# Kernel optimization log

Hardware: AMD Instinct MI355X
Metric: run time of the kernel (lower is better)

The kernel has to match this reference:

```python
import jax, jax.numpy as jnp
import numpy as np


def setup_inputs() -> dict:
    key = jax.random.key(0)
    k1, k2 = jax.random.split(key)
    inputs = jax.random.normal(k1, (4, 128, 64, 64), dtype=jnp.float32)
    # binary hole mask (1 = known background, 0 = hole), broadcast over channels
    mask = jnp.round(jax.random.uniform(k2, (4, 1, 64, 64), dtype=jnp.float32))
    return {"inputs": inputs, "mask": mask}


def reference(inputs, mask):
    # SFFA contextual attention with 1x1 dynamic kernels.
    # Note: in the original torch code the 1x1 conv with padding=1 produces
    # border scores that conv_transpose2d with padding=1 crops away exactly,
    # so the math reduces to per-pixel matmul + softmax + matmul.
    bz, nc, h, w = inputs.shape
    N = h * w
    background = inputs * mask                              # [b, c, h, w]
    # dynamic kernels: one nc-dim vector per background pixel (patch)
    K = background.reshape(bz, nc, N).transpose(0, 2, 1) + 1e-7   # [b, N, c]
    Kn = K / jnp.sqrt(jnp.sum(K * K, axis=2, keepdims=True))      # l2-normalized
    feat = inputs.reshape(bz, nc, N)                        # [b, c, N]
    scores = jnp.einsum('bpc,bcn->bpn', Kn, feat)           # [b, N(patch), N(pixel)]
    attn = jax.nn.softmax(scores, axis=1)                   # softmax over patches p
    agg = jnp.einsum('bpc,bpn->bcn', K, attn).reshape(bz, nc, h, w)
    return background + agg * (1.0 - mask)
```

## Files before the change

kernel.cpp:

```cpp
#include <hip/hip_runtime.h>
#include <hip/hip_bf16.h>

typedef __attribute__((ext_vector_type(8))) short bf16x8;
typedef __attribute__((ext_vector_type(4))) float f32x4;

#define NPIX 4096
#define NC   128
#define RS128 0.08838834764831845f

__global__ __launch_bounds__(1024) void sffa_prep(
    const float* __restrict__ x, const float* __restrict__ mask,
    ushort* __restrict__ KnW, ushort* __restrict__ QW, ushort* __restrict__ VtW,
    float* __restrict__ s0c, int* __restrict__ pixQ, int* __restrict__ cnts,
    float* __restrict__ out)
{
    __shared__ float xs[128][69];
    __shared__ float ms[64];
    __shared__ float rinv[64];
    __shared__ float ssum[64];
    __shared__ float2 part[16][64];
    __shared__ int se[64];
    __shared__ int bgn[64];
    __shared__ int tinfo[2];
    __shared__ int wredP[16], wredT[16];
    const int tid = threadIdx.x;
    const int b = blockIdx.x >> 6, nblk = blockIdx.x & 63;
    const int n0 = nblk * 64;
    const float* xb = x + (size_t)b * NC * NPIX;
    float* ob = out + (size_t)b * NC * NPIX;

    #pragma unroll
    for (int it = 0; it < 2; ++it) {
        int e4 = it * 1024 + tid;
        int c = e4 >> 4, n4 = (e4 & 15) * 4;
        float4 v = *(const float4*)(xb + (size_t)c * NPIX + n0 + n4);
        xs[c][n4+0] = v.x; xs[c][n4+1] = v.y; xs[c][n4+2] = v.z; xs[c][n4+3] = v.w;
        *(float4*)(ob + (size_t)c * NPIX + n0 + n4) = v;
    }
    if (tid < 16) {
        float4 mv = *(const float4*)(mask + (size_t)b * NPIX + n0 + tid * 4);
        ms[tid*4+0] = mv.x; ms[tid*4+1] = mv.y; ms[tid*4+2] = mv.z; ms[tid*4+3] = mv.w;
    }
    {
        const int lane = tid & 63, w = tid >> 6;
        float4 mv = *(const float4*)(mask + (size_t)b * NPIX + tid * 4);
        int f0 = mv.x < 0.5f ? 0x10000 : 1;
        int f1 = mv.y < 0.5f ? 0x10000 : 1;
        int f2 = mv.z < 0.5f ? 0x10000 : 1;
        int f3 = mv.w < 0.5f ? 0x10000 : 1;
        int p0 = tid * 4;
        int pre = 0, tot = f0 + f1 + f2 + f3;
        if (p0 + 0 < n0) pre += f0;
        if (p0 + 1 < n0) pre += f1;
        if (p0 + 2 < n0) pre += f2;
        if (p0 + 3 < n0) pre += f3;
        #pragma unroll
        for (int d = 1; d < 64; d <<= 1) {
            pre += __shfl_xor(pre, d);
            tot += __shfl_xor(tot, d);
        }
        if (lane == 0) { wredP[w] = pre; wredT[w] = tot; }
    }
    __syncthreads();
    if (tid < 64) {
        int vP = (tid < 16) ? wredP[tid] : 0;
        int vT = (tid < 16) ? wredT[tid] : 0;
        #pragma unroll
        for (int d = 1; d < 16; d <<= 1) {
            vP += __shfl_xor(vP, d);
            vT += __shfl_xor(vT, d);
        }
        int base  = __shfl(vP, 0);
        int total = __shfl(vT, 0);
        if (tid == 0 && nblk == 0) {
            cnts[b * 2]     = total & 0xffff;
            cnts[b * 2 + 1] = total >> 16;
        }
        int f = ms[tid] > 0.5f ? 1 : 0x10000;
        int s = f;
        #pragma unroll
        for (int d = 1; d < 64; d <<= 1) {
            int t = __shfl_up(s, d);
            if (tid >= d) s += t;
        }
        se[tid] = base + s - f;
    }
    __syncthreads();
    {
        int p = tid & 63, qd = tid >> 6;
        float m = ms[p];
        float s2 = 0.f, s1 = 0.f;
        #pragma unroll
        for (int i = 0; i < 8; ++i) {
            float xv = xs[qd*8 + i][p];
            float k = fmaf(xv, m, 1e-7f);
            s2 = fmaf(k, k, s2);
            s1 += xv;
        }
        part[qd][p] = make_float2(s2, s1);
    }
    __syncthreads();
    if (tid < 64) {
        float s2 = 0.f, s1 = 0.f;
        #pragma unroll
        for (int k = 0; k < 16; ++k) { float2 t = part[k][tid]; s2 += t.x; s1 += t.y; }
        rinv[tid] = rsqrtf(s2);
        ssum[tid] = s1 * RS128;
    }
    __syncthreads();
    #pragma unroll
    for (int it = 0; it < 4; ++it) {
        int e2 = it * 1024 + tid;
        int n = e2 >> 6, cp = (e2 & 63) * 2;
        int pe = se[n];
        float x0 = xs[cp][n], x1 = xs[cp+1][n];
        if (ms[n] > 0.5f) {
            int slot = pe & 0xffff;
            float k0 = x0 + 1e-7f, k1 = x1 + 1e-7f;
            float r = rinv[n];
            __hip_bfloat162 kn;
            kn.x = __float2bfloat16(k0 * r); kn.y = __float2bfloat16(k1 * r);
            *(__hip_bfloat162*)(KnW + ((size_t)b * NPIX + slot) * NC + cp) = kn;
        } else {
            int slot = pe >> 16;
            __hip_bfloat162 q;
            q.x = __float2bfloat16(x0); q.y = __float2bfloat16(x1);
            *(__hip_bfloat162*)(QW + ((size_t)b * NPIX + slot) * NC + cp) = q;
        }
    }
    if (tid < 64) {
        if (ms[tid] < 0.5f) {
            int slot = se[tid] >> 16;
            s0c [(size_t)b * NPIX + slot] = ssum[tid];
            pixQ[(size_t)b * NPIX + slot] = n0 + tid;
        } else {
            bgn[(se[tid] & 0xffff) - (se[0] & 0xffff)] = tid;
        }
    }
    if (tid == 0) {
        tinfo[0] = se[0] & 0xffff;
        tinfo[1] = (se[63] & 0xffff) + (ms[63] > 0.5f ? 1 : 0) - (se[0] & 0xffff);
    }
    __syncthreads();
    {
        const int s0b = tinfo[0], nbg = tinfo[1];
        const int j = tid & 63, cg = tid >> 6;
        if (j < nbg) {
            int n = bgn[j];
            ushort* vcol = VtW + (size_t)b * NC * NPIX + s0b + j;
            #pragma unroll
            for (int cc = 0; cc < 8; ++cc) {
                int c = cg * 8 + cc;
                __hip_bfloat16 h = __float2bfloat16(xs[c][n] + 1e-7f);
                vcol[(size_t)c * NPIX] = *(ushort*)&h;
            }
        }
    }
}

#define L_BUF 32768
#define L_P   65536
#define L_ML  75776
#define L_SZ  76800

__global__ __launch_bounds__(512, 4) void sffa_attn(
    const ushort* __restrict__ KnW, const ushort* __restrict__ QW,
    const ushort* __restrict__ VtW, const int* __restrict__ cnts,
    ushort* __restrict__ partW, float* __restrict__ mlW, int KS)
{
    __shared__ __align__(16) char smem[L_SZ];
    const int tid  = threadIdx.x;
    const int w = tid >> 6, lane = tid & 63;
    const int l15 = lane & 15, g = lane >> 4;
    const int bx = (int)blockIdx.x;
    const int per = 64 * KS;
    const int b = bx / per;
    const int rem = bx - b * per;
    const int qblk = rem / KS, ks = rem - (rem / KS) * KS;
    const int q0 = qblk * 64;
    const int cntK = cnts[b * 2], cntQ = cnts[b * 2 + 1];
    if (q0 >= cntQ) return;
    const int blk = (b * 64 + qblk) * KS + ks;

    const int nk64 = (cntK + 63) >> 6;
    const int tpk  = (nk64 + KS - 1) / KS;
    const int t0   = ks * tpk;
    const int t1   = min(t0 + tpk, nk64);
    const int NTK  = t1 - t0;

    if (NTK <= 0) {
        unsigned* pz = (unsigned*)(partW + (size_t)blk * 8192);
        #pragma unroll
        for (int i = 0; i < 8; ++i) pz[i * 512 + tid] = 0u;
        if (tid < 64)
            *(float2*)(mlW + ((size_t)blk * 64 + tid) * 2) = make_float2(-1e30f, 0.f);
        return;
    }

    const int half = w >> 2;
    const int wq   = w & 3;
    const int kbase = t0 * 64;

    const ushort* Knb = KnW + (size_t)b * NPIX * NC;
    const ushort* Qb  = QW  + (size_t)b * NPIX * NC + (size_t)q0 * NC;
    const ushort* Vtb = VtW + (size_t)b * NC * NPIX;

    #pragma unroll
    for (int it = 0; it < 2; ++it) {
        int L = (it * 512 + tid) * 16;
        int row = L >> 8, col = L & 255;
        int4 v = *(const int4*)((const char*)Qb + L);
        *(int4*)(smem + row * 256 + (col ^ ((row & 15) << 4))) = v;
    }
    __syncthreads();
    bf16x8 qf[4];
    {
        int qrow = wq * 16 + l15;
        #pragma unroll
        for (int kc = 0; kc < 4; ++kc)
            qf[kc] = *(const bf16x8*)(smem + qrow * 256 + ((64*kc + 16*g) ^ (l15 << 4)));
    }
    __syncthreads();

    const int kOff = (tid >> 4) * 256 + (((tid & 15) * 16) ^ (((tid >> 4) & 15) << 4));
    const int cV = tid >> 3, sV = tid & 7;
    const int vOff = cV * 128 + ((sV * 16) ^ ((cV & 7) << 4));
    const int4* kgbase = (const int4*)(Knb + (size_t)kbase * NC);
    const ushort* vgbase = Vtb + (size_t)cV * NPIX + kbase + sV * 8;

    int4 pr0, pr1, pr2, pr3;
    pr0 = kgbase[tid]; pr1 = kgbase[512 + tid];
    pr2 = *(const int4*)(vgbase);
    pr3 = *(const int4*)(vgbase + (size_t)64 * NPIX);
    {
        char* base = smem;
        *(int4*)(base + kOff) = pr0;
        *(int4*)(base + kOff + 8192) = pr1;
        *(int4*)(base + 16384 + vOff) = pr2;
        *(int4*)(base + 16384 + vOff + 8192) = pr3;
    }
    if (NTK > 1) {
        pr0 = kgbase[1024 + tid]; pr1 = kgbase[1536 + tid];
        pr2 = *(const int4*)(vgbase + 64);
        pr3 = *(const int4*)(vgbase + (size_t)64 * NPIX + 64);
    }
    __syncthreads();

    f32x4 acc[8];
    const f32x4 fzero = {0.f, 0.f, 0.f, 0.f};
    #pragma unroll
    for (int i = 0; i < 8; ++i) acc[i] = fzero;
    float mrun = -1e30f, lrun = 0.f;
    char* Pw = smem + L_P + w * 1280;

    for (int kt = 0; kt < NTK; ++kt) {
        if (kt + 1 < NTK) {
            char* base = smem + ((kt + 1) & 1) * L_BUF;
            *(int4*)(base + kOff) = pr0;
            *(int4*)(base + kOff + 8192) = pr1;
            *(int4*)(base + 16384 + vOff) = pr2;
            *(int4*)(base + 16384 + vOff + 8192) = pr3;
        }
        if (kt + 2 < NTK) {
            pr0 = kgbase[(kt + 2) * 1024 + tid];
            pr1 = kgbase[(kt + 2) * 1024 + 512 + tid];
            pr2 = *(const int4*)(vgbase + (kt + 2) * 64);
            pr3 = *(const int4*)(vgbase + (size_t)64 * NPIX + (kt + 2) * 64);
        }
        char* bb = smem + (kt & 1) * L_BUF;
        f32x4 sa0 = fzero, sa1 = fzero;
        {
            const char* rb0 = bb + (half * 32 + l15) * 256;
            const char* rb1 = rb0 + 4096;
            const int sw = l15 << 4;
            __builtin_amdgcn_s_setprio(1);
            #pragma unroll
            for (int kc = 0; kc < 4; ++kc) {
                int off = (64 * kc + 16 * g) ^ sw;
                bf16x8 a0 = *(const bf16x8*)(rb0 + off);
                bf16x8 a1 = *(const bf16x8*)(rb1 + off);
                sa0 = __builtin_amdgcn_mfma_f32_16x16x32_bf16(a0, qf[kc], sa0, 0, 0, 0);
                sa1 = __builtin_amdgcn_mfma_f32_16x16x32_bf16(a1, qf[kc], sa1, 0, 0, 0);
            }
            __builtin_amdgcn_s_setprio(0);
        }
        {
            int kg0 = (t0 + kt) * 64;
            if (kg0 + 64 > cntK) {
                int kb = cntK - kg0;
                int kr = half * 32 + 4 * g;
                #pragma unroll
                for (int r = 0; r < 4; ++r) {
                    if (kr + r >= kb)      sa0[r] = -3e38f;
                    if (kr + 16 + r >= kb) sa1[r] = -3e38f;
                }
            }
        }
        float tmax = fmaxf(fmaxf(fmaxf(sa0[0], sa0[1]), fmaxf(sa0[2], sa0[3])),
                           fmaxf(fmaxf(sa1[0], sa1[1]), fmaxf(sa1[2], sa1[3])));
        tmax = fmaxf(tmax, __shfl_xor(tmax, 16));
        tmax = fmaxf(tmax, __shfl_xor(tmax, 32));
        bool grow = !__all(tmax <= mrun + 8.f);
        float mnew = grow ? fmaxf(mrun, tmax) : mrun;
        float p0[4], p1[4];
        float ts = 0.f;
        #pragma unroll
        for (int r = 0; r < 4; ++r) { p0[r] = __expf(sa0[r] - mnew); ts += p0[r]; }
        #pragma unroll
        for (int r = 0; r < 4; ++r) { p1[r] = __expf(sa1[r] - mnew); ts += p1[r]; }
        ts += __shfl_xor(ts, 16);
        ts += __shfl_xor(ts, 32);
        if (grow) {
            float sc = __expf(mrun - mnew);
            lrun = lrun * sc + ts;
            float scr[4];
            #pragma unroll
            for (int r = 0; r < 4; ++r) scr[r] = __shfl(sc, 4 * g + r);
            #pragma unroll
            for (int ct = 0; ct < 8; ++ct) {
                acc[ct][0] *= scr[0]; acc[ct][1] *= scr[1];
                acc[ct][2] *= scr[2]; acc[ct][3] *= scr[3];
            }
            mrun = mnew;
        } else {
            lrun += ts;
        }
        union { __hip_bfloat162 h; unsigned u; } ua0, ua1, ub0, ub1;
        ua0.h.x = __float2bfloat16(p0[0]); ua0.h.y = __float2bfloat16(p0[1]);
        ua1.h.x = __float2bfloat16(p0[2]); ua1.h.y = __float2bfloat16(p0[3]);
        ub0.h.x = __float2bfloat16(p1[0]); ub0.h.y = __float2bfloat16(p1[1]);
        ub1.h.x = __float2bfloat16(p1[2]); ub1.h.y = __float2bfloat16(p1[3]);
        *(int2*)(Pw + l15 * 80 +      8 * g) = make_int2((int)ua0.u, (int)ua1.u);
        *(int2*)(Pw + l15 * 80 + 32 + 8 * g) = make_int2((int)ub0.u, (int)ub1.u);
        bf16x8 pf = *(const bf16x8*)(Pw + l15 * 80 + 16 * g);
        {
            const char* vb = bb + 16384;
            __builtin_amdgcn_s_setprio(1);
            #pragma unroll
            for (int ct = 0; ct < 8; ++ct) {
                int c = 16 * ct + l15;
                bf16x8 vf = *(const bf16x8*)(vb + c * 128 +
                                             ((64 * half + 16 * g) ^ ((c & 7) << 4)));
                acc[ct] = __builtin_amdgcn_mfma_f32_16x16x32_bf16(pf, vf, acc[ct], 0, 0, 0);
            }
            __builtin_amdgcn_s_setprio(0);
        }
        __syncthreads();
    }

    float* ma = (float*)(smem + L_ML);
    float* la = ma + 64; float* mb = la + 64; float* lb = mb + 64;
    const int q = wq * 16 + l15;
    if (g == 0) {
        if (half == 0) { ma[q] = mrun; la[q] = lrun; }
        else           { mb[q] = mrun; lb[q] = lrun; }
    }
    __syncthreads();
    float* agg = (float*)smem;
    {
        float mstar = fmaxf(ma[q], mb[q]);
        float f = __expf(mrun - mstar);
        float fr[4];
        #pragma unroll
        for (int r = 0; r < 4; ++r) fr[r] = __shfl(f, 4 * g + r);
        if (half == 1) {
            #pragma unroll
            for (int ct = 0; ct < 8; ++ct) {
                int c = 16 * ct + l15;
                #pragma unroll
                for (int r = 0; r < 4; ++r)
                    agg[c * 68 + wq * 16 + 4 * g + r] = acc[ct][r] * fr[r];
            }
        }
        __syncthreads();
        if (half == 0) {
            #pragma unroll
            for (int ct = 0; ct < 8; ++ct) {
                int c = 16 * ct + l15;
                #pragma unroll
                for (int r = 0; r < 4; ++r) {
                    int idx = c * 68 + wq * 16 + 4 * g + r;
                    agg[idx] = acc[ct][r] * fr[r] + agg[idx];
                }
            }
        }
    }
    __syncthreads();
    if (tid < 64) {
        float M = fmaxf(ma[tid], mb[tid]);
        float ls = la[tid] * __expf(ma[tid] - M) + lb[tid] * __expf(mb[tid] - M);
        *(float2*)(mlW + ((size_t)blk * 64 + tid) * 2) = make_float2(M, ls);
    }
    ushort* pdst = partW + (size_t)blk * 8192;
    #pragma unroll
    for (int it = 0; it < 8; ++it) {
        int idx = it * 512 + tid;
        int c = idx >> 5, n2 = (idx & 31) * 2;
        __hip_bfloat162 h;
        h.x = __float2bfloat16(agg[c * 68 + n2]);
        h.y = __float2bfloat16(agg[c * 68 + n2 + 1]);
        *(__hip_bfloat162*)(pdst + c * 64 + n2) = h;
    }
}

__global__ __launch_bounds__(256) void sffa_comb(
    const ushort* __restrict__ partW, const float* __restrict__ mlW,
    const float* __restrict__ s0c, const int* __restrict__ pixQ,
    const int* __restrict__ cnts, float* __restrict__ out, int KS)
{
    __shared__ float wgtL[4][64];
    __shared__ int pixnL[64];
    const int tid = threadIdx.x;
    const int bx = blockIdx.x;
    const int b = bx >> 8, qb = (bx >> 2) & 63, ch = bx & 3;
    const int cntK = cnts[b * 2], cntQ = cnts[b * 2 + 1];
    if (qb * 64 >= cntQ) return;
    const int blkbase = (b * 64 + qb) * KS;
    const float m0f = (float)(NPIX - cntK);

    if (tid < 64) {
        int slot = qb * 64 + tid;
        int pix = -1;
        if (slot < cntQ) {
            pix = pixQ[(size_t)b * NPIX + slot];
            float s0 = s0c[(size_t)b * NPIX + slot];
            float M = s0;
            float2 mls[4];
            #pragma unroll
            for (int k = 0; k < 4; ++k) {
                if (k < KS) {
                    mls[k] = *(const float2*)(mlW + ((size_t)(blkbase + k) * 64 + tid) * 2);
                    M = fmaxf(M, mls[k].x);
                }
            }
            float L = m0f * __expf(s0 - M);
            #pragma unroll
            for (int k = 0; k < 4; ++k)
                if (k < KS) L += mls[k].y * __expf(mls[k].x - M);
            float Li = 1.f / L;
            #pragma unroll
            for (int k = 0; k < 4; ++k)
                if (k < KS) wgtL[k][tid] = __expf(mls[k].x - M) * Li;
        }
        pixnL[tid] = pix;
    }
    __syncthreads();

    float* ob = out + (size_t)b * NC * NPIX;
    const ushort* pb = partW + (size_t)blkbase * 8192;
    {
        int cl = tid >> 3, grp = tid & 7;
        int c = ch * 32 + cl;
        float v[8] = {0.f,0.f,0.f,0.f,0.f,0.f,0.f,0.f};
        #pragma unroll
        for (int k = 0; k < 4; ++k) {
            if (k < KS) {
                ushort u[8];
                *(int4*)u = *(const int4*)(pb + (size_t)k * 8192 + c * 64 + grp * 8);
                #pragma unroll
                for (int j = 0; j < 8; ++j)
                    v[j] = fmaf(__uint_as_float((unsigned)u[j] << 16),
                                wgtL[k][grp * 8 + j], v[j]);
            }
        }
        #pragma unroll
        for (int j = 0; j < 8; ++j) {
            int pix = pixnL[grp * 8 + j];
            if (pix >= 0) ob[(size_t)c * NPIX + pix] = v[j];
        }
    }
}

extern "C" void kernel_launch(void* const* d_in, const int* in_sizes, int n_in,
                              void* d_out, int out_size, void* d_ws, size_t ws_size,
                              hipStream_t stream) {
    const float* x    = (const float*)d_in[0];
    const float* mask = (const float*)d_in[1];
    char* ws = (char*)d_ws;
    const size_t MBy = 1024 * 1024;
    const size_t KBy = 1024;

    ushort* KnW = (ushort*)(ws);
    ushort* QW  = (ushort*)(ws + 4 * MBy);
    ushort* VtW = (ushort*)(ws + 8 * MBy);

    size_t need4 = 12 * MBy + 4 * 4 * MBy + 1 * MBy;
    int KS = (ws_size >= need4) ? 4 : 2;
    ushort* partW = (ushort*)(ws + 12 * MBy);
    char* tail = ws + 12 * MBy + (size_t)KS * 4 * MBy;
    float* mlW    = (float*)(tail);
    float* s0c    = (float*)(tail + 576 * KBy);
    int*   pixQ   = (int*)(tail + 640 * KBy);
    int*   cnts   = (int*)(tail + 704 * KBy);

    sffa_prep <<<256, 1024, 0, stream>>>(x, mask, KnW, QW, VtW, s0c, pixQ, cnts,
                                         (float*)d_out);
    sffa_attn <<<4 * 64 * KS, 512, 0, stream>>>(KnW, QW, VtW, cnts, partW, mlW, KS);
    sffa_comb <<<4 * 64 * 4, 256, 0, stream>>>(partW, mlW, s0c, pixQ, cnts,
                                               (float*)d_out, KS);
}
```

Before: 53.38 us.

## Halve attention query tile to 32 rows, single-buffer LDS, 256-thread blocks

The attention kernel now handles 32 queries per block with 256 threads instead of 64 queries with 512. It replaces the double-buffered K/V shared memory with a single buffer refilled from registers after a barrier, and loads Q fragments straight from global memory without staging them in LDS. The goal is to cut LDS use roughly in half and double the block count, so more blocks fit per CU and the 256 CUs are better filled. The cost is that each K/V tile is loaded by twice as many blocks, and there is an extra barrier per tile with no overlap between the LDS write and compute. The combine kernel is reshaped to match the 32-query partials.

```diff
diff --git a/kernel.cpp b/kernel.cpp
--- a/kernel.cpp
+++ b/kernel.cpp
@@ -158,12 +158,12 @@
     }
 }
 
-#define L_BUF 32768
-#define L_P   65536
-#define L_ML  75776
-#define L_SZ  76800
-
-__global__ __launch_bounds__(512, 4) void sffa_attn(
+#define L_V   16384
+#define L_P   32768
+#define L_ML  37888
+#define L_SZ  38400
+
+__global__ __launch_bounds__(256, 4) void sffa_attn(
     const ushort* __restrict__ KnW, const ushort* __restrict__ QW,
     const ushort* __restrict__ VtW, const int* __restrict__ cnts,
     ushort* __restrict__ partW, float* __restrict__ mlW, int KS)
@@ -173,78 +173,71 @@
     const int w = tid >> 6, lane = tid & 63;
     const int l15 = lane & 15, g = lane >> 4;
     const int bx = (int)blockIdx.x;
-    const int per = 64 * KS;
+    const int per = 128 * KS;
     const int b = bx / per;
     const int rem = bx - b * per;
     const int qblk = rem / KS, ks = rem - (rem / KS) * KS;
-    const int q0 = qblk * 64;
+    const int q0 = qblk * 32;
     const int cntK = cnts[b * 2], cntQ = cnts[b * 2 + 1];
     if (q0 >= cntQ) return;
-    const int blk = (b * 64 + qblk) * KS + ks;
+    const int blk = (b * 128 + qblk) * KS + ks;
 
     const int nk64 = (cntK + 63) >> 6;
     const int tpk  = (nk64 + KS - 1) / KS;
     const int t0   = ks * tpk;
-    const int t1   = min(t0 + tpk, nk64);
-    const int NTK  = t1 - t0;
+    const int NTK  = min(t0 + tpk, nk64) - t0;
 
     if (NTK <= 0) {
-        unsigned* pz = (unsigned*)(partW + (size_t)blk * 8192);
-        #pragma unroll
-        for (int i = 0; i < 8; ++i) pz[i * 512 + tid] = 0u;
-        if (tid < 64)
-            *(float2*)(mlW + ((size_t)blk * 64 + tid) * 2) = make_float2(-1e30f, 0.f);
+        int4 z = {0,0,0,0};
+        int4* pz = (int4*)(partW + (size_t)blk * 4096);
+        pz[tid] = z; pz[256 + tid] = z;
+        if (tid < 32)
+            *(float2*)(mlW + ((size_t)blk * 32 + tid) * 2) = make_float2(-1e30f, 0.f);
         return;
     }
 
-    const int half = w >> 2;
-    const int wq   = w & 3;
+    const int wq = w & 1;
+    const int kh = w >> 1;
     const int kbase = t0 * 64;
 
     const ushort* Knb = KnW + (size_t)b * NPIX * NC;
-    const ushort* Qb  = QW  + (size_t)b * NPIX * NC + (size_t)q0 * NC;
     const ushort* Vtb = VtW + (size_t)b * NC * NPIX;
 
-    #pragma unroll
-    for (int it = 0; it < 2; ++it) {
-        int L = (it * 512 + tid) * 16;
-        int row = L >> 8, col = L & 255;
-        int4 v = *(const int4*)((const char*)Qb + L);
-        *(int4*)(smem + row * 256 + (col ^ ((row & 15) << 4))) = v;
-    }
-    __syncthreads();
     bf16x8 qf[4];
     {
-        int qrow = wq * 16 + l15;
+        const ushort* Qrow = QW + ((size_t)b * NPIX + q0 + wq * 16 + l15) * NC;
         #pragma unroll
         for (int kc = 0; kc < 4; ++kc)
-            qf[kc] = *(const bf16x8*)(smem + qrow * 256 + ((64*kc + 16*g) ^ (l15 << 4)));
-    }
-    __syncthreads();
+            qf[kc] = *(const bf16x8*)(Qrow + 32 * kc + 8 * g);
+    }
 
     const int kOff = (tid >> 4) * 256 + (((tid & 15) * 16) ^ (((tid >> 4) & 15) << 4));
-    const int cV = tid >> 3, sV = tid & 7;
-    const int vOff = cV * 128 + ((sV * 16) ^ ((cV & 7) << 4));
-    const int4* kgbase = (const int4*)(Knb + (size_t)kbase * NC);
-    const ushort* vgbase = Vtb + (size_t)cV * NPIX + kbase + sV * 8;
-
-    int4 pr0, pr1, pr2, pr3;
-    pr0 = kgbase[tid]; pr1 = kgbase[512 + tid];
-    pr2 = *(const int4*)(vgbase);
-    pr3 = *(const int4*)(vgbase + (size_t)64 * NPIX);
-    {
-        char* base = smem;
-        *(int4*)(base + kOff) = pr0;
-        *(int4*)(base + kOff + 8192) = pr1;
-        *(int4*)(base + 16384 + vOff) = pr2;
-        *(int4*)(base + 16384 + vOff + 8192) = pr3;
-    }
+    const int vOff = (tid >> 3) * 128 + (((tid & 7) * 16) ^ (((tid >> 3) & 7) << 4));
+    const int4* kg = (const int4*)(Knb + (size_t)kbase * NC);
+    const ushort* vg = Vtb + (size_t)(tid >> 3) * NPIX + kbase + (tid & 7) * 8;
+
+    int4 prK0, prK1, prK2, prK3, prV0, prV1, prV2, prV3;
+    prK0 = kg[tid]; prK1 = kg[256+tid]; prK2 = kg[512+tid]; prK3 = kg[768+tid];
+    prV0 = *(const int4*)(vg);
+    prV1 = *(const int4*)(vg + (size_t)32 * NPIX);
+    prV2 = *(const int4*)(vg + (size_t)64 * NPIX);
+    prV3 = *(const int4*)(vg + (size_t)96 * NPIX);
+    *(int4*)(smem + kOff)          = prK0;
+    *(int4*)(smem + kOff + 4096)   = prK1;
+    *(int4*)(smem + kOff + 8192)   = prK2;
+    *(int4*)(smem + kOff + 12288)  = prK3;
+    *(int4*)(smem + L_V + vOff)         = prV0;
+    *(int4*)(smem + L_V + vOff + 4096)  = prV1;
+    *(int4*)(smem + L_V + vOff + 8192)  = prV2;
+    *(int4*)(smem + L_V + vOff + 12288) = prV3;
+    __syncthreads();
     if (NTK > 1) {
-        pr0 = kgbase[1024 + tid]; pr1 = kgbase[1536 + tid];
-        pr2 = *(const int4*)(vgbase + 64);
-        pr3 = *(const int4*)(vgbase + (size_t)64 * NPIX + 64);
-    }
-    __syncthreads();
+        prK0 = kg[1024+tid]; prK1 = kg[1280+tid]; prK2 = kg[1536+tid]; prK3 = kg[1792+tid];
+        prV0 = *(const int4*)(vg + 64);
+        prV1 = *(const int4*)(vg + (size_t)32 * NPIX + 64);
+        prV2 = *(const int4*)(vg + (size_t)64 * NPIX + 64);
+        prV3 = *(const int4*)(vg + (size_t)96 * NPIX + 64);
+    }
 
     f32x4 acc[8];
     const f32x4 fzero = {0.f, 0.f, 0.f, 0.f};
@@ -254,23 +247,9 @@
     char* Pw = smem + L_P + w * 1280;
 
     for (int kt = 0; kt < NTK; ++kt) {
-        if (kt + 1 < NTK) {
-            char* base = smem + ((kt + 1) & 1) * L_BUF;
-            *(int4*)(base + kOff) = pr0;
-            *(int4*)(base + kOff + 8192) = pr1;
-            *(int4*)(base + 16384 + vOff) = pr2;
-            *(int4*)(base + 16384 + vOff + 8192) = pr3;
-        }
-        if (kt + 2 < NTK) {
-            pr0 = kgbase[(kt + 2) * 1024 + tid];
-            pr1 = kgbase[(kt + 2) * 1024 + 512 + tid];
-            pr2 = *(const int4*)(vgbase + (kt + 2) * 64);
-            pr3 = *(const int4*)(vgbase + (size_t)64 * NPIX + (kt + 2) * 64);
-        }
-        char* bb = smem + (kt & 1) * L_BUF;
         f32x4 sa0 = fzero, sa1 = fzero;
         {
-            const char* rb0 = bb + (half * 32 + l15) * 256;
+            const char* rb0 = smem + (kh * 32 + l15) * 256;
             const char* rb1 = rb0 + 4096;
             const int sw = l15 << 4;
             __builtin_amdgcn_s_setprio(1);
@@ -288,7 +267,7 @@
             int kg0 = (t0 + kt) * 64;
             if (kg0 + 64 > cntK) {
                 int kb = cntK - kg0;
-                int kr = half * 32 + 4 * g;
+                int kr = kh * 32 + 4 * g;
                 #pragma unroll
                 for (int r = 0; r < 4; ++r) {
                     if (kr + r >= kb)      sa0[r] = -3e38f;
@@ -334,72 +313,90 @@
         *(int2*)(Pw + l15 * 80 + 32 + 8 * g) = make_int2((int)ub0.u, (int)ub1.u);
         bf16x8 pf = *(const bf16x8*)(Pw + l15 * 80 + 16 * g);
         {
-            const char* vb = bb + 16384;
+            const char* bv = smem + L_V;
             __builtin_amdgcn_s_setprio(1);
             #pragma unroll
             for (int ct = 0; ct < 8; ++ct) {
                 int c = 16 * ct + l15;
-                bf16x8 vf = *(const bf16x8*)(vb + c * 128 +
-                                             ((64 * half + 16 * g) ^ ((c & 7) << 4)));
+                bf16x8 vf = *(const bf16x8*)(bv + c * 128 +
+                                             ((64 * kh + 16 * g) ^ ((c & 7) << 4)));
                 acc[ct] = __builtin_amdgcn_mfma_f32_16x16x32_bf16(pf, vf, acc[ct], 0, 0, 0);
             }
             __builtin_amdgcn_s_setprio(0);
         }
         __syncthreads();
+        if (kt + 1 < NTK) {
+            *(int4*)(smem + kOff)          = prK0;
+            *(int4*)(smem + kOff + 4096)   = prK1;
+            *(int4*)(smem + kOff + 8192)   = prK2;
+            *(int4*)(smem + kOff + 12288)  = prK3;
+            *(int4*)(smem + L_V + vOff)         = prV0;
+            *(int4*)(smem + L_V + vOff + 4096)  = prV1;
+            *(int4*)(smem + L_V + vOff + 8192)  = prV2;
+            *(int4*)(smem + L_V + vOff + 12288) = prV3;
+            __syncthreads();
+            if (kt + 2 < NTK) {
+                int tb = (kt + 2) * 1024;
+                prK0 = kg[tb+tid]; prK1 = kg[tb+256+tid];
+                prK2 = kg[tb+512+tid]; prK3 = kg[tb+768+tid];
+                const ushort* vgk = vg + (kt + 2) * 64;
+                prV0 = *(const int4*)(vgk);
+                prV1 = *(const int4*)(vgk + (size_t)32 * NPIX);
+                prV2 = *(const int4*)(vgk + (size_t)64 * NPIX);
+                prV3 = *(const int4*)(vgk + (size_t)96 * NPIX);
+            }
+        }
     }
 
     float* ma = (float*)(smem + L_ML);
-    float* la = ma + 64; float* mb = la + 64; float* lb = mb + 64;
-    const int q = wq * 16 + l15;
-    if (g == 0) {
-        if (half == 0) { ma[q] = mrun; la[q] = lrun; }
-        else           { mb[q] = mrun; lb[q] = lrun; }
-    }
+    float* la = ma + 64;
+    const int qs = wq * 16 + l15;
+    if (g == 0) { ma[kh * 32 + qs] = mrun; la[kh * 32 + qs] = lrun; }
     __syncthreads();
     float* agg = (float*)smem;
     {
-        float mstar = fmaxf(ma[q], mb[q]);
+        float mstar = fmaxf(ma[qs], ma[32 + qs]);
         float f = __expf(mrun - mstar);
         float fr[4];
         #pragma unroll
         for (int r = 0; r < 4; ++r) fr[r] = __shfl(f, 4 * g + r);
-        if (half == 1) {
+        if (kh == 1) {
             #pragma unroll
             for (int ct = 0; ct < 8; ++ct) {
                 int c = 16 * ct + l15;
                 #pragma unroll
                 for (int r = 0; r < 4; ++r)
-                    agg[c * 68 + wq * 16 + 4 * g + r] = acc[ct][r] * fr[r];
+                    agg[c * 36 + wq * 16 + 4 * g + r] = acc[ct][r] * fr[r];
             }
         }
         __syncthreads();
-        if (half == 0) {
+        if (kh == 0) {
             #pragma unroll
             for (int ct = 0; ct < 8; ++ct) {
                 int c = 16 * ct + l15;
                 #pragma unroll
                 for (int r = 0; r < 4; ++r) {
-                    int idx = c * 68 + wq * 16 + 4 * g + r;
+                    int idx = c * 36 + wq * 16 + 4 * g + r;
                     agg[idx] = acc[ct][r] * fr[r] + agg[idx];
                 }
             }
         }
     }
     __syncthreads();
-    if (tid < 64) {
-        float M = fmaxf(ma[tid], mb[tid]);
-        float ls = la[tid] * __expf(ma[tid] - M) + lb[tid] * __expf(mb[tid] - M);
-        *(float2*)(mlW + ((size_t)blk * 64 + tid) * 2) = make_float2(M, ls);
-    }
-    ushort* pdst = partW + (size_t)blk * 8192;
+    if (tid < 32) {
+        float M = fmaxf(ma[tid], ma[32 + tid]);
+        float ls = la[tid] * __expf(ma[tid] - M) + la[32 + tid] * __expf(ma[32 + tid] - M);
+        *(float2*)(mlW + ((size_t)blk * 32 + tid) * 2) = make_float2(M, ls);
+    }
+    ushort* pdst = partW + (size_t)blk * 4096;
     #pragma unroll
     for (int it = 0; it < 8; ++it) {
-        int idx = it * 512 + tid;
-        int c = idx >> 5, n2 = (idx & 31) * 2;
+        int idx = it * 256 + tid;
+        int c = idx >> 4, n2 = (idx & 15) * 2;
         __hip_bfloat162 h;
-        h.x = __float2bfloat16(agg[c * 68 + n2]);
-        h.y = __float2bfloat16(agg[c * 68 + n2 + 1]);
-        *(__hip_bfloat162*)(pdst + c * 64 + n2) = h;
+        h.x = __float2bfloat16(agg[c * 36 + n2]);
+        h.y = __float2bfloat16(agg[c * 36 + n2 + 1]);
+        *(__hip_bfloat162*)(pdst + c * 32 + n2) = h;
     }
 }
 
@@ -408,18 +405,18 @@
     const float* __restrict__ s0c, const int* __restrict__ pixQ,
     const int* __restrict__ cnts, float* __restrict__ out, int KS)
 {
-    __shared__ float wgtL[4][64];
-    __shared__ int pixnL[64];
+    __shared__ float wgtL[4][32];
+    __shared__ int pixnL[32];
     const int tid = threadIdx.x;
     const int bx = blockIdx.x;
-    const int b = bx >> 8, qb = (bx >> 2) & 63, ch = bx & 3;
+    const int b = bx >> 7, qb = bx & 127;
     const int cntK = cnts[b * 2], cntQ = cnts[b * 2 + 1];
-    if (qb * 64 >= cntQ) return;
-    const int blkbase = (b * 64 + qb) * KS;
+    if (qb * 32 >= cntQ) return;
+    const int blkbase = (b * 128 + qb) * KS;
     const float m0f = (float)(NPIX - cntK);
 
-    if (tid < 64) {
-        int slot = qb * 64 + tid;
+    if (tid < 32) {
+        int slot = qb * 32 + tid;
         int pix = -1;
         if (slot < cntQ) {
             pix = pixQ[(size_t)b * NPIX + slot];
@@ -429,7 +426,7 @@
             #pragma unroll
             for (int k = 0; k < 4; ++k) {
                 if (k < KS) {
-                    mls[k] = *(const float2*)(mlW + ((size_t)(blkbase + k) * 64 + tid) * 2);
+                    mls[k] = *(const float2*)(mlW + ((size_t)(blkbase + k) * 32 + tid) * 2);
                     M = fmaxf(M, mls[k].x);
                 }
             }
@@ -447,25 +444,27 @@
     __syncthreads();
 
     float* ob = out + (size_t)b * NC * NPIX;
-    const ushort* pb = partW + (size_t)blkbase * 8192;
+    const ushort* pb = partW + (size_t)blkbase * 4096;
     {
-        int cl = tid >> 3, grp = tid & 7;
-        int c = ch * 32 + cl;
-        float v[8] = {0.f,0.f,0.f,0.f,0.f,0.f,0.f,0.f};
+        int c = tid >> 1, grp = tid & 1;
+        float v[16];
+        #pragma unroll
+        for (int j = 0; j < 16; ++j) v[j] = 0.f;
         #pragma unroll
         for (int k = 0; k < 4; ++k) {
             if (k < KS) {
-                ushort u[8];
-                *(int4*)u = *(const int4*)(pb + (size_t)k * 8192 + c * 64 + grp * 8);
+                ushort u[16];
+                *(int4*)(u)     = *(const int4*)(pb + (size_t)k * 4096 + c * 32 + grp * 16);
+                *(int4*)(u + 8) = *(const int4*)(pb + (size_t)k * 4096 + c * 32 + grp * 16 + 8);
                 #pragma unroll
-                for (int j = 0; j < 8; ++j)
+                for (int j = 0; j < 16; ++j)
                     v[j] = fmaf(__uint_as_float((unsigned)u[j] << 16),
-                                wgtL[k][grp * 8 + j], v[j]);
-            }
-        }
-        #pragma unroll
-        for (int j = 0; j < 8; ++j) {
-            int pix = pixnL[grp * 8 + j];
+                                wgtL[k][grp * 16 + j], v[j]);
+            }
+        }
+        #pragma unroll
+        for (int j = 0; j < 16; ++j) {
+            int pix = pixnL[grp * 16 + j];
             if (pix >= 0) ob[(size_t)c * NPIX + pix] = v[j];
         }
     }
@@ -484,18 +483,18 @@
     ushort* QW  = (ushort*)(ws + 4 * MBy);
     ushort* VtW = (ushort*)(ws + 8 * MBy);
 
-    size_t need4 = 12 * MBy + 4 * 4 * MBy + 1 * MBy;
+    size_t need4 = 12 * MBy + 16 * MBy + 1 * MBy;
     int KS = (ws_size >= need4) ? 4 : 2;
     ushort* partW = (ushort*)(ws + 12 * MBy);
     char* tail = ws + 12 * MBy + (size_t)KS * 4 * MBy;
-    float* mlW    = (float*)(tail);
-    float* s0c    = (float*)(tail + 576 * KBy);
-    int*   pixQ   = (int*)(tail + 640 * KBy);
-    int*   cnts   = (int*)(tail + 704 * KBy);
+    float* mlW  = (float*)(tail);
+    float* s0c  = (float*)(tail + 576 * KBy);
+    int*   pixQ = (int*)(tail + 640 * KBy);
+    int*   cnts = (int*)(tail + 704 * KBy);
 
     sffa_prep <<<256, 1024, 0, stream>>>(x, mask, KnW, QW, VtW, s0c, pixQ, cnts,
                                          (float*)d_out);
-    sffa_attn <<<4 * 64 * KS, 512, 0, stream>>>(KnW, QW, VtW, cnts, partW, mlW, KS);
-    sffa_comb <<<4 * 64 * 4, 256, 0, stream>>>(partW, mlW, s0c, pixQ, cnts,
-                                               (float*)d_out, KS);
+    sffa_attn <<<4 * 128 * KS, 256, 0, stream>>>(KnW, QW, VtW, cnts, partW, mlW, KS);
+    sffa_comb <<<4 * 128, 256, 0, stream>>>(partW, mlW, s0c, pixQ, cnts,
+                                            (float*)d_out, KS);
 }
```

Measured after the change: 62.23 us. 1.17x slower.

## Stream K/V tiles via direct global-to-LDS loads and load Q fragments directly

Applied to the files above, without the earlier changes.

The attention kernel now uses global_load_lds to move K and V tiles straight into LDS, with the XOR swizzle moved onto the source address so the LDS layout is unchanged. This replaces the register-staged prefetch and its two-tile lookahead. Q fragments are read directly from global memory instead of going through LDS with two extra barriers. The combine kernel now launches half as many blocks, each handling 64 channels over two iterations. This cuts register pressure and VGPR-to-LDS store instructions, but loses the deeper prefetch distance and depends on async load ordering being covered by the existing barriers.

```diff
diff --git a/kernel.cpp b/kernel.cpp
--- a/kernel.cpp
+++ b/kernel.cpp
@@ -7,6 +7,10 @@
 #define NPIX 4096
 #define NC   128
 #define RS128 0.08838834764831845f
+
+#define GL2LDS(g, l) __builtin_amdgcn_global_load_lds( \
+    (const __attribute__((address_space(1))) void*)(g), \
+    (__attribute__((address_space(3))) void*)(l), 16, 0, 0)
 
 __global__ __launch_bounds__(1024) void sffa_prep(
     const float* __restrict__ x, const float* __restrict__ mask,
@@ -185,8 +189,7 @@
     const int nk64 = (cntK + 63) >> 6;
     const int tpk  = (nk64 + KS - 1) / KS;
     const int t0   = ks * tpk;
-    const int t1   = min(t0 + tpk, nk64);
-    const int NTK  = t1 - t0;
+    const int NTK  = min(t0 + tpk, nk64) - t0;
 
     if (NTK <= 0) {
         unsigned* pz = (unsigned*)(partW + (size_t)blk * 8192);
@@ -202,48 +205,28 @@
     const int kbase = t0 * 64;
 
     const ushort* Knb = KnW + (size_t)b * NPIX * NC;
-    const ushort* Qb  = QW  + (size_t)b * NPIX * NC + (size_t)q0 * NC;
     const ushort* Vtb = VtW + (size_t)b * NC * NPIX;
 
-    #pragma unroll
-    for (int it = 0; it < 2; ++it) {
-        int L = (it * 512 + tid) * 16;
-        int row = L >> 8, col = L & 255;
-        int4 v = *(const int4*)((const char*)Qb + L);
-        *(int4*)(smem + row * 256 + (col ^ ((row & 15) << 4))) = v;
-    }
-    __syncthreads();
     bf16x8 qf[4];
     {
-        int qrow = wq * 16 + l15;
+        const ushort* Qrow = QW + ((size_t)b * NPIX + q0 + wq * 16 + l15) * NC;
         #pragma unroll
         for (int kc = 0; kc < 4; ++kc)
-            qf[kc] = *(const bf16x8*)(smem + qrow * 256 + ((64*kc + 16*g) ^ (l15 << 4)));
-    }
-    __syncthreads();
-
-    const int kOff = (tid >> 4) * 256 + (((tid & 15) * 16) ^ (((tid >> 4) & 15) << 4));
-    const int cV = tid >> 3, sV = tid & 7;
-    const int vOff = cV * 128 + ((sV * 16) ^ ((cV & 7) << 4));
-    const int4* kgbase = (const int4*)(Knb + (size_t)kbase * NC);
-    const ushort* vgbase = Vtb + (size_t)cV * NPIX + kbase + sV * 8;
-
-    int4 pr0, pr1, pr2, pr3;
-    pr0 = kgbase[tid]; pr1 = kgbase[512 + tid];
-    pr2 = *(const int4*)(vgbase);
-    pr3 = *(const int4*)(vgbase + (size_t)64 * NPIX);
-    {
-        char* base = smem;
-        *(int4*)(base + kOff) = pr0;
-        *(int4*)(base + kOff + 8192) = pr1;
-        *(int4*)(base + 16384 + vOff) = pr2;
-        *(int4*)(base + 16384 + vOff + 8192) = pr3;
-    }
-    if (NTK > 1) {
-        pr0 = kgbase[1024 + tid]; pr1 = kgbase[1536 + tid];
-        pr2 = *(const int4*)(vgbase + 64);
-        pr3 = *(const int4*)(vgbase + (size_t)64 * NPIX + 64);
-    }
+            qf[kc] = *(const bf16x8*)(Qrow + 32 * kc + 8 * g);
+    }
+
+    const int rK = tid >> 4;
+    const char* srcK = (const char*)(Knb + (size_t)(kbase + rK) * NC)
+                     + (((tid & 15) ^ (rK & 15)) << 4);
+    const int rV = tid >> 3;
+    const char* srcV = (const char*)(Vtb + (size_t)rV * NPIX + kbase)
+                     + (((tid & 7) ^ (rV & 7)) << 4);
+    char* d0 = smem + tid * 16;
+
+    GL2LDS(srcK,        d0);
+    GL2LDS(srcK + 8192, d0 + 8192);
+    GL2LDS(srcV,                           d0 + 16384);
+    GL2LDS(srcV + (size_t)64 * NPIX * 2,   d0 + 24576);
     __syncthreads();
 
     f32x4 acc[8];
@@ -255,17 +238,13 @@
 
     for (int kt = 0; kt < NTK; ++kt) {
         if (kt + 1 < NTK) {
-            char* base = smem + ((kt + 1) & 1) * L_BUF;
-            *(int4*)(base + kOff) = pr0;
-            *(int4*)(base + kOff + 8192) = pr1;
-            *(int4*)(base + 16384 + vOff) = pr2;
-            *(int4*)(base + 16384 + vOff + 8192) = pr3;
-        }
-        if (kt + 2 < NTK) {
-            pr0 = kgbase[(kt + 2) * 1024 + tid];
-            pr1 = kgbase[(kt + 2) * 1024 + 512 + tid];
-            pr2 = *(const int4*)(vgbase + (kt + 2) * 64);
-            pr3 = *(const int4*)(vgbase + (size_t)64 * NPIX + (kt + 2) * 64);
+            char* nb = smem + ((kt + 1) & 1) * L_BUF + tid * 16;
+            const char* sK = srcK + (size_t)(kt + 1) * 16384;
+            const char* sV = srcV + (size_t)(kt + 1) * 128;
+            GL2LDS(sK,        nb);
+            GL2LDS(sK + 8192, nb + 8192);
+            GL2LDS(sV,                         nb + 16384);
+            GL2LDS(sV + (size_t)64 * NPIX * 2, nb + 24576);
         }
         char* bb = smem + (kt & 1) * L_BUF;
         f32x4 sa0 = fzero, sa1 = fzero;
@@ -412,7 +391,7 @@
     __shared__ int pixnL[64];
     const int tid = threadIdx.x;
     const int bx = blockIdx.x;
-    const int b = bx >> 8, qb = (bx >> 2) & 63, ch = bx & 3;
+    const int b = bx >> 7, qb = (bx >> 1) & 63, ch = bx & 1;
     const int cntK = cnts[b * 2], cntQ = cnts[b * 2 + 1];
     if (qb * 64 >= cntQ) return;
     const int blkbase = (b * 64 + qb) * KS;
@@ -446,11 +425,12 @@
     }
     __syncthreads();
 
-    float* ob = out + (size_t)b * NC * NPIX;
-    const ushort* pb = partW + (size_t)blkbase * 8192;
-    {
-        int cl = tid >> 3, grp = tid & 7;
-        int c = ch * 32 + cl;
+    float* ob = out + ((size_t)b * NC + ch * 64) * NPIX;
+    const ushort* pb = partW + (size_t)blkbase * 8192 + ch * 4096;
+    #pragma unroll
+    for (int it = 0; it < 2; ++it) {
+        int idx = it * 256 + tid;
+        int c = idx >> 3, grp = idx & 7;
         float v[8] = {0.f,0.f,0.f,0.f,0.f,0.f,0.f,0.f};
         #pragma unroll
         for (int k = 0; k < 4; ++k) {
@@ -484,18 +464,18 @@
     ushort* QW  = (ushort*)(ws + 4 * MBy);
     ushort* VtW = (ushort*)(ws + 8 * MBy);
 
-    size_t need4 = 12 * MBy + 4 * 4 * MBy + 1 * MBy;
+    size_t need4 = 12 * MBy + 16 * MBy + 1 * MBy;
     int KS = (ws_size >= need4) ? 4 : 2;
     ushort* partW = (ushort*)(ws + 12 * MBy);
     char* tail = ws + 12 * MBy + (size_t)KS * 4 * MBy;
-    float* mlW    = (float*)(tail);
-    float* s0c    = (float*)(tail + 576 * KBy);
-    int*   pixQ   = (int*)(tail + 640 * KBy);
-    int*   cnts   = (int*)(tail + 704 * KBy);
+    float* mlW  = (float*)(tail);
+    float* s0c  = (float*)(tail + 576 * KBy);
+    int*   pixQ = (int*)(tail + 640 * KBy);
+    int*   cnts = (int*)(tail + 704 * KBy);
 
     sffa_prep <<<256, 1024, 0, stream>>>(x, mask, KnW, QW, VtW, s0c, pixQ, cnts,
                                          (float*)d_out);
     sffa_attn <<<4 * 64 * KS, 512, 0, stream>>>(KnW, QW, VtW, cnts, partW, mlW, KS);
-    sffa_comb <<<4 * 64 * 4, 256, 0, stream>>>(partW, mlW, s0c, pixQ, cnts,
-                                               (float*)d_out, KS);
+    sffa_comb <<<4 * 128, 256, 0, stream>>>(partW, mlW, s0c, pixQ, cnts,
+                                            (float*)d_out, KS);
 }
```

New measurement: 54.56 us. 2.2% more time.
